# Kernel optimization log

Measured on AMD Instinct MI355X. Metric: run time of the kernel, lower is better.

## Reference

```python
import jax, jax.numpy as jnp
import numpy as np

EPS = 1e-6


def setup_inputs() -> dict:
    key = jax.random.key(0)
    kx, kw = jax.random.split(key)
    B, C, N = 8, 256, 2048
    x = jax.random.normal(kx, (B, C, N), dtype=jnp.float32)
    # nn.Linear(dim*2, 2, bias=False): weight shape [2, 2*C]
    W = jax.random.normal(kw, (2, 2 * C), dtype=jnp.float32) * (1.0 / np.sqrt(2 * C))
    return {"x": x, "W": W}


def reference(x, W):
    B, C, N = x.shape
    # cosine similarity matrix [B, N, N]
    sim = jnp.einsum('bcn,bcm->bnm', x, x)
    # torch: sqrt(sum(x^2 + 1e-6, dim=1)) -> eps added per-channel before sum
    norms = jnp.sqrt(jnp.sum(x * x + EPS, axis=1))            # [B, N]
    io_abs = sim / (norms[:, :, None] * norms[:, None, :])    # [B, N, N]
    # zero the diagonal (fill_diagonal_(0)) before argmax
    io_abs = io_abs * (1.0 - jnp.eye(N, dtype=io_abs.dtype))
    idx = jnp.argmax(io_abs, axis=2)                          # [B, N] nearest-neighbor per token
    # gather retrieved features: f_re[b, :, n] = x[b, :, idx[b, n]]
    f_re = jnp.take_along_axis(x, idx[:, None, :], axis=2)    # [B, C, N]
    # gated fusion
    fus = jnp.concatenate([x, f_re], axis=1).transpose(0, 2, 1)  # [B, N, 2C]
    w = jax.nn.softmax(fus @ W.T, axis=-1)                    # [B, N, 2]
    w = w.transpose(0, 2, 1)                                  # [B, 2, N]
    out = x * w[:, 0:1, :] + f_re * w[:, 1:2, :]
    return (out, f_re)
```

## Files before the change

### kernel.cpp

```cpp
#include <hip/hip_runtime.h>
#include <hip/hip_bf16.h>
#include <math.h>

constexpr int B_ = 8;
constexpr int C_ = 256;
constexpr int N_ = 2048;
constexpr int CN_ = C_ * N_;
constexpr int TOT_ = B_ * C_ * N_;
constexpr int BN_ = B_ * N_;
constexpr int NTILES = 16;
constexpr int NPAIRS = 136;
constexpr float EPSC = 256.0f * 1e-6f;

typedef __attribute__((ext_vector_type(8))) short bf16x8;
typedef __attribute__((ext_vector_type(4))) float f32x4;

__device__ __forceinline__ void g2l16(const void* g, void* l) {
    __builtin_amdgcn_global_load_lds(
        (const __attribute__((address_space(1))) void*)g,
        (__attribute__((address_space(3))) void*)l, 16, 0, 0);
}

__device__ __forceinline__ unsigned short bits(__hip_bfloat16 h) {
    union { __hip_bfloat16 b; unsigned short u; } cv;
    cv.b = h;
    return cv.u;
}

__device__ __forceinline__ float b2f(short s) {
    union { float f; unsigned u; } cv;
    cv.u = ((unsigned)(unsigned short)s) << 16;
    return cv.f;
}

__device__ __forceinline__ unsigned long long packkey(float v, int m) {
    const unsigned b = __float_as_uint(v);
    const unsigned u = (b & 0x80000000u) ? ~b : (b | 0x80000000u);
    return ((unsigned long long)u << 32) | (unsigned)(2047 - m);
}

__device__ __forceinline__ float rnorm4(const float* __restrict__ normp, int idx) {
    return 1.0f / sqrtf(normp[idx] + normp[BN_ + idx] + normp[2 * BN_ + idx] +
                        normp[3 * BN_ + idx] + EPSC);
}

__global__ __launch_bounds__(256) void convert_kernel(const float* __restrict__ x,
                                                      __hip_bfloat16* __restrict__ hiT,
                                                      __hip_bfloat16* __restrict__ loT,
                                                      float* __restrict__ normp,
                                                      int* __restrict__ rcnt) {
    const int blk = blockIdx.x;
    const int batch = blk & 7;
    const int nt = (blk >> 3) & 31;
    const int ctile = blk >> 8;
    const int n0 = nt << 6, c0 = ctile << 6;
    const int t = threadIdx.x;
    const int i = t & 63, j = t >> 6;

    if (blk == 0 && t == 0) rcnt[0] = 0;

    __shared__ float tb[64][65];
    __shared__ float red[4][64];

    float s = 0.f;
    const float* xp = x + (size_t)batch * CN_ + (size_t)c0 * N_ + n0 + i;
#pragma unroll 4
    for (int r = 0; r < 16; ++r) {
        const int cl = j + r * 4;
        const float v = xp[(size_t)cl * N_];
        tb[cl][i] = v;
        s += v * v;
    }
    red[j][i] = s;
    __syncthreads();

    const int cp = t & 31;
    const int c2 = cp << 1;
    const int nb = t >> 5;
#pragma unroll 4
    for (int r = 0; r < 8; ++r) {
        const int n = nb + r * 8;
        const float v0 = tb[c2][n], v1 = tb[c2 + 1][n];
        const size_t o = ((size_t)batch * N_ + n0 + n) * C_ + c0 + c2;
        const __hip_bfloat16 h0 = __float2bfloat16(v0);
        const __hip_bfloat16 h1 = __float2bfloat16(v1);
        const __hip_bfloat16 g0 = __float2bfloat16(v0 - __bfloat162float(h0));
        const __hip_bfloat16 g1 = __float2bfloat16(v1 - __bfloat162float(h1));
        ((unsigned*)hiT)[o >> 1] = ((unsigned)bits(h1) << 16) | bits(h0);
        ((unsigned*)loT)[o >> 1] = ((unsigned)bits(g1) << 16) | bits(g0);
    }
    if (j == 0) {
        const float tt = red[0][i] + red[1][i] + red[2][i] + red[3][i];
        normp[ctile * BN_ + batch * N_ + n0 + i] = tt;
    }
}

__global__ __launch_bounds__(512) void gram_mfma_kernel(
        const __hip_bfloat16* __restrict__ hiT, const __hip_bfloat16* __restrict__ loT,
        const float* __restrict__ normp,
        float* __restrict__ pval, int* __restrict__ pidx, float* __restrict__ pval2) {
    const int blk = blockIdx.x;
    const int batch = blk & 7;
    int p = blk >> 3;
    int bn = 0;
    while (p >= NTILES - bn) { p -= NTILES - bn; ++bn; }
    const int bm = bn + p;
    const bool diag = (bn == bm);
    const int n0 = bn << 7, m0 = bm << 7;

    __shared__ short As0[128 * 64];
    __shared__ short As1[128 * 64];
    __shared__ short Bs0[128 * 64];
    __shared__ short Bs1[128 * 64];
    short* ov = &As0[0];
    float (*rv1)[4] = (float(*)[4])(ov + 0);
    int (*ri1)[4] = (int(*)[4])(ov + 1024);
    float (*rv2)[4] = (float(*)[4])(ov + 2048);
    float (*cv1)[2] = (float(*)[2])(ov + 3072);
    int (*ci1)[2] = (int(*)[2])(ov + 3584);
    float (*cv2)[2] = (float(*)[2])(ov + 4096);
    float* rnA = (float*)(ov + 4608);

    const int tid = threadIdx.x;
    const int l = tid & 63, w = tid >> 6;
    const int lm = l & 15, q = l >> 4;
    const int x7 = lm & 7;
    const int wn = (w >> 2) << 6;
    const int wm = (w & 3) << 5;

    const size_t bbase = (size_t)batch * CN_;
    const short* gA[2];
    const short* gB[2];
    int ldsoff[2];
#pragma unroll
    for (int pp = 0; pp < 2; ++pp) {
        const int slot = tid + pp * 512;
        const int r = slot >> 3, sidx = slot & 7;
        const int sw = sidx ^ (r & 7);
        const short* base = (const short*)((sw < 4) ? hiT : loT);
        gA[pp] = base + bbase + (size_t)(n0 + r) * C_ + (sw & 3) * 8;
        gB[pp] = base + bbase + (size_t)(m0 + r) * C_ + (sw & 3) * 8;
        ldsoff[pp] = slot * 8;
    }
    int aoff[8], boff[4];
#pragma unroll
    for (int rt = 0; rt < 4; ++rt) {
        const int ra = wn + rt * 16 + lm;
        aoff[rt * 2] = ra * 64 + ((q ^ x7) * 8);
        aoff[rt * 2 + 1] = ra * 64 + (((4 | q) ^ x7) * 8);
    }
#pragma unroll
    for (int ct = 0; ct < 2; ++ct) {
        const int rb = wm + ct * 16 + lm;
        boff[ct * 2] = rb * 64 + ((q ^ x7) * 8);
        boff[ct * 2 + 1] = rb * 64 + (((4 | q) ^ x7) * 8);
    }

    f32x4 acc[4][2];
#pragma unroll
    for (int rt = 0; rt < 4; ++rt)
#pragma unroll
        for (int ct = 0; ct < 2; ++ct) acc[rt][ct] = (f32x4){0.f, 0.f, 0.f, 0.f};

#pragma unroll
    for (int pp = 0; pp < 2; ++pp) {
        g2l16(gA[pp], As0 + ldsoff[pp]);
        g2l16(gB[pp], Bs0 + ldsoff[pp]);
    }
    __syncthreads();

#pragma unroll
    for (int kt = 0; kt < 8; ++kt) {
        short* Ac = (kt & 1) ? As1 : As0;
        short* Bc = (kt & 1) ? Bs1 : Bs0;
        if (kt < 7) {
            short* An = (kt & 1) ? As0 : As1;
            short* Bn = (kt & 1) ? Bs0 : Bs1;
#pragma unroll
            for (int pp = 0; pp < 2; ++pp) {
                g2l16(gA[pp] + (kt + 1) * 32, An + ldsoff[pp]);
                g2l16(gB[pp] + (kt + 1) * 32, Bn + ldsoff[pp]);
            }
        }
        bf16x8 ah[4], al[4], bh[2], bl[2];
#pragma unroll
        for (int rt = 0; rt < 4; ++rt) {
            ah[rt] = *(const bf16x8*)(Ac + aoff[rt * 2]);
            al[rt] = *(const bf16x8*)(Ac + aoff[rt * 2 + 1]);
        }
#pragma unroll
        for (int ct = 0; ct < 2; ++ct) {
            bh[ct] = *(const bf16x8*)(Bc + boff[ct * 2]);
            bl[ct] = *(const bf16x8*)(Bc + boff[ct * 2 + 1]);
        }
#pragma unroll
        for (int rt = 0; rt < 4; ++rt)
#pragma unroll
            for (int ct = 0; ct < 2; ++ct) {
                acc[rt][ct] = __builtin_amdgcn_mfma_f32_16x16x32_bf16(
                    ah[rt], bh[ct], acc[rt][ct], 0, 0, 0);
                acc[rt][ct] = __builtin_amdgcn_mfma_f32_16x16x32_bf16(
                    ah[rt], bl[ct], acc[rt][ct], 0, 0, 0);
                acc[rt][ct] = __builtin_amdgcn_mfma_f32_16x16x32_bf16(
                    al[rt], bh[ct], acc[rt][ct], 0, 0, 0);
            }
        __syncthreads();
    }

    if (tid < 128) rnA[tid] = rnorm4(normp, batch * N_ + n0 + tid);

    float rnm[2];
#pragma unroll
    for (int ct = 0; ct < 2; ++ct)
        rnm[ct] = rnorm4(normp, batch * N_ + m0 + wm + ct * 16 + lm);

#pragma unroll
    for (int rt = 0; rt < 4; ++rt) {
#pragma unroll
        for (int r = 0; r < 4; ++r) {
            const int nrow = n0 + wn + rt * 16 + q * 4 + r;
            float v1 = -3.4e38f, v2 = -3.4e38f;
            int i1 = 0x7fffffff;
#pragma unroll
            for (int ct = 0; ct < 2; ++ct) {
                const int m = m0 + wm + ct * 16 + lm;
                const float v = acc[rt][ct][r] * rnm[ct];
                if (m == nrow) continue;
                if (v > v1) { v2 = v1; v1 = v; i1 = m; }
                else if (v > v2) v2 = v;
            }
#pragma unroll
            for (int d = 1; d < 16; d <<= 1) {
                const float ov1 = __shfl_xor(v1, d, 64);
                const int oi1 = __shfl_xor(i1, d, 64);
                const float ov2 = __shfl_xor(v2, d, 64);
                if (ov1 > v1 || (ov1 == v1 && oi1 < i1)) {
                    v2 = fmaxf(v1, ov2); v1 = ov1; i1 = oi1;
                } else {
                    v2 = fmaxf(v2, ov1);
                }
            }
            if (lm == 0) {
                const int rloc = wn + rt * 16 + q * 4 + r;
                rv1[rloc][w & 3] = v1;
                ri1[rloc][w & 3] = i1;
                rv2[rloc][w & 3] = v2;
            }
        }
    }
    __syncthreads();

    if (!diag) {
        float rnn[4][4];
#pragma unroll
        for (int rt = 0; rt < 4; ++rt)
#pragma unroll
            for (int r = 0; r < 4; ++r) rnn[rt][r] = rnA[wn + rt * 16 + q * 4 + r];
#pragma unroll
        for (int ct = 0; ct < 2; ++ct) {
            float v1 = -3.4e38f, v2 = -3.4e38f;
            int i1 = 0x7fffffff;
#pragma unroll
            for (int rt = 0; rt < 4; ++rt) {
#pragma unroll
                for (int r = 0; r < 4; ++r) {
                    const float v = acc[rt][ct][r] * rnn[rt][r];
                    const int nn = n0 + wn + rt * 16 + q * 4 + r;
                    if (v > v1) { v2 = v1; v1 = v; i1 = nn; }
                    else if (v > v2) v2 = v;
                }
            }
#pragma unroll
            for (int d = 16; d < 64; d <<= 1) {
                const float ov1 = __shfl_xor(v1, d, 64);
                const int oi1 = __shfl_xor(i1, d, 64);
                const float ov2 = __shfl_xor(v2, d, 64);
                if (ov1 > v1 || (ov1 == v1 && oi1 < i1)) {
                    v2 = fmaxf(v1, ov2); v1 = ov1; i1 = oi1;
                } else {
                    v2 = fmaxf(v2, ov1);
                }
            }
            if (q == 0) {
                const int mloc = wm + ct * 16 + lm;
                cv1[mloc][w >> 2] = v1;
                ci1[mloc][w >> 2] = i1;
                cv2[mloc][w >> 2] = v2;
            }
        }
    }
    __syncthreads();

    if (tid < 128) {
        {
            float v1 = rv1[tid][0]; int i1 = ri1[tid][0]; float v2 = rv2[tid][0];
#pragma unroll
            for (int s = 1; s < 4; ++s) {
                const float ov1 = rv1[tid][s]; const int oi1 = ri1[tid][s]; const float ov2 = rv2[tid][s];
                if (ov1 > v1 || (ov1 == v1 && oi1 < i1)) { v2 = fmaxf(v1, ov2); v1 = ov1; i1 = oi1; }
                else v2 = fmaxf(v2, ov1);
            }
            const size_t gi = (size_t)(batch * NTILES + bm) * N_ + n0 + tid;
            pval[gi] = v1; pidx[gi] = i1; pval2[gi] = v2;
        }
        if (!diag) {
            float v1 = cv1[tid][0]; int i1 = ci1[tid][0]; float v2 = cv2[tid][0];
            const float ov1 = cv1[tid][1]; const int oi1 = ci1[tid][1]; const float ov2 = cv2[tid][1];
            if (ov1 > v1 || (ov1 == v1 && oi1 < i1)) { v2 = fmaxf(v1, ov2); v1 = ov1; i1 = oi1; }
            else v2 = fmaxf(v2, ov1);
            const size_t gi = (size_t)(batch * NTILES + bn) * N_ + m0 + tid;
            pval[gi] = v1; pidx[gi] = i1; pval2[gi] = v2;
        }
    }
}

__global__ void combine_kernel(const float* __restrict__ pval, const int* __restrict__ pidx,
                               const float* __restrict__ pval2, int* __restrict__ fidx,
                               int* __restrict__ rcnt, int* __restrict__ ridx,
                               unsigned long long* __restrict__ pbest) {
    const int t = blockIdx.x * 256 + threadIdx.x;
    const int batch = t >> 11, n = t & 2047;
    float v1 = -3.4e38f, v2 = -3.4e38f;
    int i1 = 0x7fffffff;
    for (int s = 0; s < NTILES; ++s) {
        const size_t gi = (size_t)(batch * NTILES + s) * N_ + n;
        const float ov1 = pval[gi]; const int oi1 = pidx[gi]; const float ov2 = pval2[gi];
        if (ov1 > v1 || (ov1 == v1 && oi1 < i1)) { v2 = fmaxf(v1, ov2); v1 = ov1; i1 = oi1; }
        else v2 = fmaxf(v2, ov1);
    }
    fidx[t] = i1;
    if (v1 - v2 < 1e-4f) {
        const int slot = atomicAdd(rcnt, 1);
        ridx[slot] = t;
        pbest[slot] = 0ull;
    }
}

__global__ __launch_bounds__(256) void rescue_kernel(const float* __restrict__ x,
                                                     const float* __restrict__ normp,
                                                     const int* __restrict__ rcnt,
                                                     const int* __restrict__ ridx,
                                                     unsigned long long* __restrict__ pbest) {
    const int cnt = *rcnt;
    const int nwork = cnt << 3;
    const int tid = threadIdx.x;
    __shared__ unsigned long long bk[256];
    for (int wi = blockIdx.x; wi < nwork; wi += gridDim.x) {
        const int rr = wi >> 3, ch = wi & 7;
        const int t = ridx[rr];
        const int batch = t >> 11, n = t & 2047;
        const int m = (ch << 8) + tid;
        const float* xb = x + (size_t)batch * CN_;
        float s0 = 0.f, s1 = 0.f, s2 = 0.f, s3 = 0.f;
        const float* xn = xb + n;
        const float* xm = xb + m;
#pragma unroll 4
        for (int c = 0; c < C_; c += 4) {
            s0 += xn[(size_t)(c + 0) * N_] * xm[(size_t)(c + 0) * N_];
            s1 += xn[(size_t)(c + 1) * N_] * xm[(size_t)(c + 1) * N_];
            s2 += xn[(size_t)(c + 2) * N_] * xm[(size_t)(c + 2) * N_];
            s3 += xn[(size_t)(c + 3) * N_] * xm[(size_t)(c + 3) * N_];
        }
        const float v = ((s0 + s1) + (s2 + s3)) * rnorm4(normp, batch * N_ + m);
        bk[tid] = (m == n) ? 0ull : packkey(v, m);
        __syncthreads();
        for (int sft = 128; sft > 0; sft >>= 1) {
            if (tid < sft) {
                const unsigned long long o = bk[tid + sft];
                if (o > bk[tid]) bk[tid] = o;
            }
            __syncthreads();
        }
        if (tid == 0) atomicMax(&pbest[rr], bk[0]);
        __syncthreads();
    }
}

__global__ __launch_bounds__(512) void finish_kernel(const float* __restrict__ x,
                                                     const __hip_bfloat16* __restrict__ hiT,
                                                     const __hip_bfloat16* __restrict__ loT,
                                                     const float* __restrict__ W,
                                                     const int* __restrict__ fidx,
                                                     const int* __restrict__ rcnt,
                                                     const int* __restrict__ ridx,
                                                     const unsigned long long* __restrict__ pbest,
                                                     float* __restrict__ out) {
    const int batch = blockIdx.x & 7;
    const int nt = blockIdx.x >> 3;
    const int n0 = nt << 6;
    const int t = threadIdx.x;
    const int lane = t & 63, cw = t >> 6;

    __shared__ float Wl[1024];
    __shared__ int il[64];
    __shared__ float pl0[8][64], pl1[8][64];
    __shared__ float w0s[64], w1s[64];

    for (int u = t; u < 1024; u += 512) Wl[u] = W[u];
    if (t < 64) il[t] = fidx[batch * N_ + n0 + t];
    __syncthreads();
    {
        const int cnt = *rcnt;
        for (int rr = t; rr < cnt; rr += 512) {
            const int tt = ridx[rr];
            if ((tt >> 11) == batch) {
                const int n = tt & 2047;
                if (n >= n0 && n < n0 + 64) {
                    const unsigned long long k = pbest[rr];
                    il[n - n0] = 2047 - (int)(unsigned)(k & 0xffffffffull);
                }
            }
        }
    }
    __syncthreads();

    const int myrow = il[lane];
    const size_t rowb = ((size_t)batch * N_ + myrow) * C_ + cw * 32;

    float fre[32];
    {
        const bf16x8* hp = (const bf16x8*)(hiT + rowb);
        const bf16x8* lp = (const bf16x8*)(loT + rowb);
#pragma unroll
        for (int v8 = 0; v8 < 4; ++v8) {
            const bf16x8 h = hp[v8];
            const bf16x8 g = lp[v8];
#pragma unroll
            for (int e = 0; e < 8; ++e) fre[v8 * 8 + e] = b2f(h[e]) + b2f(g[e]);
        }
    }

    const float* xb = x + (size_t)batch * CN_ + n0 + lane;
    float xr[32];
    float l0 = 0.f, l1 = 0.f;
#pragma unroll
    for (int cc = 0; cc < 32; ++cc) {
        const int c = cw * 32 + cc;
        const float xv = xb[(size_t)c * N_];
        xr[cc] = xv;
        l0 += xv * Wl[c] + fre[cc] * Wl[256 + c];
        l1 += xv * Wl[512 + c] + fre[cc] * Wl[768 + c];
    }
    pl0[cw][lane] = l0;
    pl1[cw][lane] = l1;
    __syncthreads();
    if (t < 64) {
        float L0 = 0.f, L1 = 0.f;
#pragma unroll
        for (int g = 0; g < 8; ++g) { L0 += pl0[g][t]; L1 += pl1[g][t]; }
        const float mx = fmaxf(L0, L1);
        const float e0 = expf(L0 - mx);
        const float e1 = expf(L1 - mx);
        const float inv = 1.0f / (e0 + e1);
        w0s[t] = e0 * inv;
        w1s[t] = e1 * inv;
    }
    __syncthreads();
    const float w0 = w0s[lane], w1 = w1s[lane];

#pragma unroll
    for (int cc = 0; cc < 32; ++cc) {
        const int c = cw * 32 + cc;
        const size_t off = (size_t)batch * CN_ + (size_t)c * N_ + n0 + lane;
        out[off] = xr[cc] * w0 + fre[cc] * w1;
        out[TOT_ + off] = fre[cc];
    }
}

extern "C" void kernel_launch(void* const* d_in, const int* in_sizes, int n_in,
                              void* d_out, int out_size, void* d_ws, size_t ws_size,
                              hipStream_t stream) {
    const float* x = (const float*)d_in[0];
    const float* W = (const float*)d_in[1];
    float* out = (float*)d_out;

    const size_t BF_BYTES = (size_t)TOT_ * 2;
    const size_t NORM_BYTES = (size_t)BN_ * 4;
    const size_t P_BYTES = (size_t)B_ * NTILES * N_ * 4;

    uint8_t* p = (uint8_t*)d_ws;
    __hip_bfloat16* hiT = (__hip_bfloat16*)p; p += BF_BYTES;
    __hip_bfloat16* loT = (__hip_bfloat16*)p; p += BF_BYTES;
    float* normp = (float*)p; p += 4 * NORM_BYTES;
    float* pval = (float*)p; p += P_BYTES;
    int* pidx = (int*)p; p += P_BYTES;
    float* pval2 = (float*)p; p += P_BYTES;
    int* fidx = (int*)p; p += NORM_BYTES;
    int* rcnt = (int*)p; p += 256;
    int* ridx = (int*)p; p += NORM_BYTES;
    unsigned long long* pbest = (unsigned long long*)p; p += (size_t)BN_ * 8;

    convert_kernel<<<1024, 256, 0, stream>>>(x, hiT, loT, normp, rcnt);
    gram_mfma_kernel<<<B_ * NPAIRS, 512, 0, stream>>>(hiT, loT, normp, pval, pidx, pval2);
    combine_kernel<<<64, 256, 0, stream>>>(pval, pidx, pval2, fidx, rcnt, ridx, pbest);
    rescue_kernel<<<256, 256, 0, stream>>>(x, normp, rcnt, ridx, pbest);
    finish_kernel<<<256, 512, 0, stream>>>(x, hiT, loT, W, fidx, rcnt, ridx, pbest, out);
}
```

Measured before the change: 174.2 us.

## Batch rescue rows per block with per-batch queues and wave-shuffle reductions

```diff
diff --git a/kernel.cpp b/kernel.cpp
--- a/kernel.cpp
+++ b/kernel.cpp
@@ -10,10 +10,13 @@
 constexpr int BN_ = B_ * N_;
 constexpr int NTILES = 16;
 constexpr int NPAIRS = 136;
+constexpr int TCAP = 2048;
+constexpr int MAXG = 128;
 constexpr float EPSC = 256.0f * 1e-6f;
 
 typedef __attribute__((ext_vector_type(8))) short bf16x8;
 typedef __attribute__((ext_vector_type(4))) float f32x4;
+typedef __attribute__((ext_vector_type(2))) unsigned int u32x2;
 
 __device__ __forceinline__ void g2l16(const void* g, void* l) {
     __builtin_amdgcn_global_load_lds(
@@ -42,6 +45,10 @@
 __device__ __forceinline__ float rnorm4(const float* __restrict__ normp, int idx) {
     return 1.0f / sqrtf(normp[idx] + normp[BN_ + idx] + normp[2 * BN_ + idx] +
                         normp[3 * BN_ + idx] + EPSC);
+}
+
+__device__ __forceinline__ unsigned packpair(float a, float b) {
+    return ((unsigned)bits(__float2bfloat16(b)) << 16) | bits(__float2bfloat16(a));
 }
 
 __global__ __launch_bounds__(256) void convert_kernel(const float* __restrict__ x,
@@ -57,7 +64,7 @@
     const int t = threadIdx.x;
     const int i = t & 63, j = t >> 6;
 
-    if (blk == 0 && t == 0) rcnt[0] = 0;
+    if (blk == 0 && t < 8) rcnt[t] = 0;
 
     __shared__ float tb[64][65];
     __shared__ float red[4][64];
@@ -74,20 +81,29 @@
     red[j][i] = s;
     __syncthreads();
 
-    const int cp = t & 31;
-    const int c2 = cp << 1;
-    const int nb = t >> 5;
-#pragma unroll 4
-    for (int r = 0; r < 8; ++r) {
-        const int n = nb + r * 8;
-        const float v0 = tb[c2][n], v1 = tb[c2 + 1][n];
-        const size_t o = ((size_t)batch * N_ + n0 + n) * C_ + c0 + c2;
+    const int cq = t & 15;
+    const int nb = t >> 4;
+#pragma unroll
+    for (int r = 0; r < 4; ++r) {
+        const int n = nb + r * 16;
+        const int c = cq << 2;
+        float v0 = tb[c][n], v1 = tb[c + 1][n], v2 = tb[c + 2][n], v3 = tb[c + 3][n];
         const __hip_bfloat16 h0 = __float2bfloat16(v0);
         const __hip_bfloat16 h1 = __float2bfloat16(v1);
-        const __hip_bfloat16 g0 = __float2bfloat16(v0 - __bfloat162float(h0));
-        const __hip_bfloat16 g1 = __float2bfloat16(v1 - __bfloat162float(h1));
-        ((unsigned*)hiT)[o >> 1] = ((unsigned)bits(h1) << 16) | bits(h0);
-        ((unsigned*)loT)[o >> 1] = ((unsigned)bits(g1) << 16) | bits(g0);
+        const __hip_bfloat16 h2 = __float2bfloat16(v2);
+        const __hip_bfloat16 h3 = __float2bfloat16(v3);
+        const float g0 = v0 - __bfloat162float(h0);
+        const float g1 = v1 - __bfloat162float(h1);
+        const float g2 = v2 - __bfloat162float(h2);
+        const float g3 = v3 - __bfloat162float(h3);
+        const size_t o = ((size_t)batch * N_ + n0 + n) * C_ + c0 + c;
+        u32x2 hp, lp;
+        hp[0] = ((unsigned)bits(h1) << 16) | bits(h0);
+        hp[1] = ((unsigned)bits(h3) << 16) | bits(h2);
+        lp[0] = packpair(g0, g1);
+        lp[1] = packpair(g2, g3);
+        ((u32x2*)hiT)[o >> 2] = hp;
+        ((u32x2*)loT)[o >> 2] = lp;
     }
     if (j == 0) {
         const float tt = red[0][i] + red[1][i] + red[2][i] + red[3][i];
@@ -330,9 +346,11 @@
     }
     fidx[t] = i1;
     if (v1 - v2 < 1e-4f) {
-        const int slot = atomicAdd(rcnt, 1);
-        ridx[slot] = t;
-        pbest[slot] = 0ull;
+        const int slot = atomicAdd(rcnt + batch, 1);
+        if (slot < TCAP) {
+            ridx[batch * TCAP + slot] = n;
+            pbest[batch * TCAP + slot] = 0ull;
+        }
     }
 }
 
@@ -341,38 +359,59 @@
                                                      const int* __restrict__ rcnt,
                                                      const int* __restrict__ ridx,
                                                      unsigned long long* __restrict__ pbest) {
-    const int cnt = *rcnt;
-    const int nwork = cnt << 3;
     const int tid = threadIdx.x;
-    __shared__ unsigned long long bk[256];
-    for (int wi = blockIdx.x; wi < nwork; wi += gridDim.x) {
-        const int rr = wi >> 3, ch = wi & 7;
-        const int t = ridx[rr];
-        const int batch = t >> 11, n = t & 2047;
+    __shared__ float xn[16][256];
+    __shared__ int nrow[16];
+    __shared__ unsigned long long wk[4][16];
+
+    for (int wi = blockIdx.x; wi < 8 * MAXG * 8; wi += gridDim.x) {
+        const int b = wi >> 10;
+        const int g = (wi >> 3) & (MAXG - 1);
+        const int ch = wi & 7;
+        const int cnt = min(rcnt[b], TCAP);
+        if (g * 16 >= cnt) continue;
+        const int nt = min(16, cnt - g * 16);
+        const float* xb = x + (size_t)b * CN_;
+
+        __syncthreads();
+        if (tid < 16) nrow[tid] = ridx[b * TCAP + g * 16 + ((tid < nt) ? tid : 0)];
+        __syncthreads();
+        {
+            const int c = tid & 255;
+            for (int j = 0; j < 16; ++j) xn[j][c] = xb[(size_t)c * N_ + nrow[j]];
+        }
+        __syncthreads();
+
         const int m = (ch << 8) + tid;
-        const float* xb = x + (size_t)batch * CN_;
-        float s0 = 0.f, s1 = 0.f, s2 = 0.f, s3 = 0.f;
-        const float* xn = xb + n;
+        float acc[16];
+#pragma unroll
+        for (int j = 0; j < 16; ++j) acc[j] = 0.f;
         const float* xm = xb + m;
-#pragma unroll 4
-        for (int c = 0; c < C_; c += 4) {
-            s0 += xn[(size_t)(c + 0) * N_] * xm[(size_t)(c + 0) * N_];
-            s1 += xn[(size_t)(c + 1) * N_] * xm[(size_t)(c + 1) * N_];
-            s2 += xn[(size_t)(c + 2) * N_] * xm[(size_t)(c + 2) * N_];
-            s3 += xn[(size_t)(c + 3) * N_] * xm[(size_t)(c + 3) * N_];
-        }
-        const float v = ((s0 + s1) + (s2 + s3)) * rnorm4(normp, batch * N_ + m);
-        bk[tid] = (m == n) ? 0ull : packkey(v, m);
+        for (int c = 0; c < C_; ++c) {
+            const float vm = xm[(size_t)c * N_];
+#pragma unroll
+            for (int j = 0; j < 16; ++j) acc[j] += vm * xn[j][c];
+        }
+        const float rn = rnorm4(normp, b * N_ + m);
+        const int w = tid >> 6;
+#pragma unroll
+        for (int j = 0; j < 16; ++j) {
+            unsigned long long k = (m == nrow[j]) ? 0ull : packkey(acc[j] * rn, m);
+#pragma unroll
+            for (int d = 1; d < 64; d <<= 1) {
+                const unsigned long long o = __shfl_xor(k, d, 64);
+                if (o > k) k = o;
+            }
+            if ((tid & 63) == 0) wk[w][j] = k;
+        }
         __syncthreads();
-        for (int sft = 128; sft > 0; sft >>= 1) {
-            if (tid < sft) {
-                const unsigned long long o = bk[tid + sft];
-                if (o > bk[tid]) bk[tid] = o;
-            }
-            __syncthreads();
-        }
-        if (tid == 0) atomicMax(&pbest[rr], bk[0]);
-        __syncthreads();
+        if (tid < 16 && tid < nt) {
+            unsigned long long k = wk[0][tid];
+            if (wk[1][tid] > k) k = wk[1][tid];
+            if (wk[2][tid] > k) k = wk[2][tid];
+            if (wk[3][tid] > k) k = wk[3][tid];
+            atomicMax(&pbest[b * TCAP + g * 16 + tid], k);
+        }
     }
 }
 
@@ -400,15 +439,12 @@
     if (t < 64) il[t] = fidx[batch * N_ + n0 + t];
     __syncthreads();
     {
-        const int cnt = *rcnt;
+        const int cnt = min(rcnt[batch], TCAP);
         for (int rr = t; rr < cnt; rr += 512) {
-            const int tt = ridx[rr];
-            if ((tt >> 11) == batch) {
-                const int n = tt & 2047;
-                if (n >= n0 && n < n0 + 64) {
-                    const unsigned long long k = pbest[rr];
-                    il[n - n0] = 2047 - (int)(unsigned)(k & 0xffffffffull);
-                }
+            const int n = ridx[batch * TCAP + rr];
+            if (n >= n0 && n < n0 + 64) {
+                const unsigned long long k = pbest[batch * TCAP + rr];
+                il[n - n0] = 2047 - (int)(unsigned)(k & 0xffffffffull);
             }
         }
     }
```

Measured after the change: 312.9 us. 1.8x slower.

## Fuse combine, rescue and finish into one cooperative kernel; vectorize bf16 split stores

Applied to the files above, without the earlier changes.

```diff
diff --git a/kernel.cpp b/kernel.cpp
--- a/kernel.cpp
+++ b/kernel.cpp
@@ -1,6 +1,9 @@
 #include <hip/hip_runtime.h>
 #include <hip/hip_bf16.h>
+#include <hip/hip_cooperative_groups.h>
 #include <math.h>
+
+namespace cg = cooperative_groups;
 
 constexpr int B_ = 8;
 constexpr int C_ = 256;
@@ -14,6 +17,7 @@
 
 typedef __attribute__((ext_vector_type(8))) short bf16x8;
 typedef __attribute__((ext_vector_type(4))) float f32x4;
+typedef __attribute__((ext_vector_type(2))) unsigned int u32x2;
 
 __device__ __forceinline__ void g2l16(const void* g, void* l) {
     __builtin_amdgcn_global_load_lds(
@@ -42,6 +46,10 @@
 __device__ __forceinline__ float rnorm4(const float* __restrict__ normp, int idx) {
     return 1.0f / sqrtf(normp[idx] + normp[BN_ + idx] + normp[2 * BN_ + idx] +
                         normp[3 * BN_ + idx] + EPSC);
+}
+
+__device__ __forceinline__ unsigned packpair(float a, float b) {
+    return ((unsigned)bits(__float2bfloat16(b)) << 16) | bits(__float2bfloat16(a));
 }
 
 __global__ __launch_bounds__(256) void convert_kernel(const float* __restrict__ x,
@@ -74,20 +82,29 @@
     red[j][i] = s;
     __syncthreads();
 
-    const int cp = t & 31;
-    const int c2 = cp << 1;
-    const int nb = t >> 5;
-#pragma unroll 4
-    for (int r = 0; r < 8; ++r) {
-        const int n = nb + r * 8;
-        const float v0 = tb[c2][n], v1 = tb[c2 + 1][n];
-        const size_t o = ((size_t)batch * N_ + n0 + n) * C_ + c0 + c2;
+    const int cq = t & 15;
+    const int nb = t >> 4;
+#pragma unroll
+    for (int r = 0; r < 4; ++r) {
+        const int n = nb + r * 16;
+        const int c = cq << 2;
+        float v0 = tb[c][n], v1 = tb[c + 1][n], v2 = tb[c + 2][n], v3 = tb[c + 3][n];
         const __hip_bfloat16 h0 = __float2bfloat16(v0);
         const __hip_bfloat16 h1 = __float2bfloat16(v1);
-        const __hip_bfloat16 g0 = __float2bfloat16(v0 - __bfloat162float(h0));
-        const __hip_bfloat16 g1 = __float2bfloat16(v1 - __bfloat162float(h1));
-        ((unsigned*)hiT)[o >> 1] = ((unsigned)bits(h1) << 16) | bits(h0);
-        ((unsigned*)loT)[o >> 1] = ((unsigned)bits(g1) << 16) | bits(g0);
+        const __hip_bfloat16 h2 = __float2bfloat16(v2);
+        const __hip_bfloat16 h3 = __float2bfloat16(v3);
+        const float g0 = v0 - __bfloat162float(h0);
+        const float g1 = v1 - __bfloat162float(h1);
+        const float g2 = v2 - __bfloat162float(h2);
+        const float g3 = v3 - __bfloat162float(h3);
+        const size_t o = ((size_t)batch * N_ + n0 + n) * C_ + c0 + c;
+        u32x2 hp, lp;
+        hp[0] = ((unsigned)bits(h1) << 16) | bits(h0);
+        hp[1] = ((unsigned)bits(h3) << 16) | bits(h2);
+        lp[0] = packpair(g0, g1);
+        lp[1] = packpair(g2, g3);
+        ((u32x2*)hiT)[o >> 2] = hp;
+        ((u32x2*)loT)[o >> 2] = lp;
     }
     if (j == 0) {
         const float tt = red[0][i] + red[1][i] + red[2][i] + red[3][i];
@@ -314,156 +331,155 @@
     }
 }
 
-__global__ void combine_kernel(const float* __restrict__ pval, const int* __restrict__ pidx,
-                               const float* __restrict__ pval2, int* __restrict__ fidx,
-                               int* __restrict__ rcnt, int* __restrict__ ridx,
-                               unsigned long long* __restrict__ pbest) {
-    const int t = blockIdx.x * 256 + threadIdx.x;
-    const int batch = t >> 11, n = t & 2047;
-    float v1 = -3.4e38f, v2 = -3.4e38f;
-    int i1 = 0x7fffffff;
-    for (int s = 0; s < NTILES; ++s) {
-        const size_t gi = (size_t)(batch * NTILES + s) * N_ + n;
-        const float ov1 = pval[gi]; const int oi1 = pidx[gi]; const float ov2 = pval2[gi];
-        if (ov1 > v1 || (ov1 == v1 && oi1 < i1)) { v2 = fmaxf(v1, ov2); v1 = ov1; i1 = oi1; }
-        else v2 = fmaxf(v2, ov1);
-    }
-    fidx[t] = i1;
-    if (v1 - v2 < 1e-4f) {
-        const int slot = atomicAdd(rcnt, 1);
-        ridx[slot] = t;
-        pbest[slot] = 0ull;
-    }
-}
-
-__global__ __launch_bounds__(256) void rescue_kernel(const float* __restrict__ x,
-                                                     const float* __restrict__ normp,
-                                                     const int* __restrict__ rcnt,
-                                                     const int* __restrict__ ridx,
-                                                     unsigned long long* __restrict__ pbest) {
-    const int cnt = *rcnt;
-    const int nwork = cnt << 3;
+__global__ __launch_bounds__(512) void tail_kernel(
+        const float* __restrict__ x,
+        const __hip_bfloat16* __restrict__ hiT, const __hip_bfloat16* __restrict__ loT,
+        const float* __restrict__ W, const float* __restrict__ normp,
+        const float* __restrict__ pval, const int* __restrict__ pidx,
+        const float* __restrict__ pval2,
+        int* __restrict__ fidx, int* __restrict__ rcnt, int* __restrict__ ridx,
+        unsigned long long* __restrict__ pbest, float* __restrict__ out) {
     const int tid = threadIdx.x;
-    __shared__ unsigned long long bk[256];
-    for (int wi = blockIdx.x; wi < nwork; wi += gridDim.x) {
-        const int rr = wi >> 3, ch = wi & 7;
-        const int t = ridx[rr];
-        const int batch = t >> 11, n = t & 2047;
-        const int m = (ch << 8) + tid;
-        const float* xb = x + (size_t)batch * CN_;
-        float s0 = 0.f, s1 = 0.f, s2 = 0.f, s3 = 0.f;
-        const float* xn = xb + n;
-        const float* xm = xb + m;
-#pragma unroll 4
-        for (int c = 0; c < C_; c += 4) {
-            s0 += xn[(size_t)(c + 0) * N_] * xm[(size_t)(c + 0) * N_];
-            s1 += xn[(size_t)(c + 1) * N_] * xm[(size_t)(c + 1) * N_];
-            s2 += xn[(size_t)(c + 2) * N_] * xm[(size_t)(c + 2) * N_];
-            s3 += xn[(size_t)(c + 3) * N_] * xm[(size_t)(c + 3) * N_];
-        }
-        const float v = ((s0 + s1) + (s2 + s3)) * rnorm4(normp, batch * N_ + m);
-        bk[tid] = (m == n) ? 0ull : packkey(v, m);
-        __syncthreads();
-        for (int sft = 128; sft > 0; sft >>= 1) {
-            if (tid < sft) {
-                const unsigned long long o = bk[tid + sft];
-                if (o > bk[tid]) bk[tid] = o;
-            }
-            __syncthreads();
-        }
-        if (tid == 0) atomicMax(&pbest[rr], bk[0]);
-        __syncthreads();
-    }
-}
-
-__global__ __launch_bounds__(512) void finish_kernel(const float* __restrict__ x,
-                                                     const __hip_bfloat16* __restrict__ hiT,
-                                                     const __hip_bfloat16* __restrict__ loT,
-                                                     const float* __restrict__ W,
-                                                     const int* __restrict__ fidx,
-                                                     const int* __restrict__ rcnt,
-                                                     const int* __restrict__ ridx,
-                                                     const unsigned long long* __restrict__ pbest,
-                                                     float* __restrict__ out) {
-    const int batch = blockIdx.x & 7;
-    const int nt = blockIdx.x >> 3;
-    const int n0 = nt << 6;
-    const int t = threadIdx.x;
-    const int lane = t & 63, cw = t >> 6;
-
+    const int blk = blockIdx.x;
+
+    __shared__ unsigned long long bk[512];
     __shared__ float Wl[1024];
     __shared__ int il[64];
     __shared__ float pl0[8][64], pl1[8][64];
     __shared__ float w0s[64], w1s[64];
 
-    for (int u = t; u < 1024; u += 512) Wl[u] = W[u];
-    if (t < 64) il[t] = fidx[batch * N_ + n0 + t];
-    __syncthreads();
+    {
+        const int t = blk * 512 + tid;
+        if (t < BN_) {
+            const int batch = t >> 11, n = t & 2047;
+            float v1 = -3.4e38f, v2 = -3.4e38f;
+            int i1 = 0x7fffffff;
+            for (int s = 0; s < NTILES; ++s) {
+                const size_t gi = (size_t)(batch * NTILES + s) * N_ + n;
+                const float ov1 = pval[gi]; const int oi1 = pidx[gi]; const float ov2 = pval2[gi];
+                if (ov1 > v1 || (ov1 == v1 && oi1 < i1)) { v2 = fmaxf(v1, ov2); v1 = ov1; i1 = oi1; }
+                else v2 = fmaxf(v2, ov1);
+            }
+            fidx[t] = i1;
+            if (v1 - v2 < 1e-4f) {
+                const int slot = atomicAdd(rcnt, 1);
+                ridx[slot] = t;
+                pbest[slot] = 0ull;
+            }
+        }
+    }
+    cg::this_grid().sync();
+
     {
         const int cnt = *rcnt;
-        for (int rr = t; rr < cnt; rr += 512) {
-            const int tt = ridx[rr];
-            if ((tt >> 11) == batch) {
-                const int n = tt & 2047;
-                if (n >= n0 && n < n0 + 64) {
-                    const unsigned long long k = pbest[rr];
-                    il[n - n0] = 2047 - (int)(unsigned)(k & 0xffffffffull);
+        const int nwork = cnt << 2;
+        for (int wi = blk; wi < nwork; wi += 256) {
+            const int rr = wi >> 2, ch = wi & 3;
+            const int t = ridx[rr];
+            const int batch = t >> 11, n = t & 2047;
+            const int m = (ch << 9) + tid;
+            const float* xb = x + (size_t)batch * CN_;
+            float s0 = 0.f, s1 = 0.f, s2 = 0.f, s3 = 0.f;
+            const float* xn = xb + n;
+            const float* xm = xb + m;
+#pragma unroll 4
+            for (int c = 0; c < C_; c += 4) {
+                s0 += xn[(size_t)(c + 0) * N_] * xm[(size_t)(c + 0) * N_];
+                s1 += xn[(size_t)(c + 1) * N_] * xm[(size_t)(c + 1) * N_];
+                s2 += xn[(size_t)(c + 2) * N_] * xm[(size_t)(c + 2) * N_];
+                s3 += xn[(size_t)(c + 3) * N_] * xm[(size_t)(c + 3) * N_];
+            }
+            const float v = ((s0 + s1) + (s2 + s3)) * rnorm4(normp, batch * N_ + m);
+            bk[tid] = (m == n) ? 0ull : packkey(v, m);
+            __syncthreads();
+            for (int sft = 256; sft > 0; sft >>= 1) {
+                if (tid < sft) {
+                    const unsigned long long o = bk[tid + sft];
+                    if (o > bk[tid]) bk[tid] = o;
                 }
-            }
-        }
-    }
-    __syncthreads();
-
-    const int myrow = il[lane];
-    const size_t rowb = ((size_t)batch * N_ + myrow) * C_ + cw * 32;
-
-    float fre[32];
+                __syncthreads();
+            }
+            if (tid == 0) atomicMax(&pbest[rr], bk[0]);
+            __syncthreads();
+        }
+    }
+    cg::this_grid().sync();
+
     {
-        const bf16x8* hp = (const bf16x8*)(hiT + rowb);
-        const bf16x8* lp = (const bf16x8*)(loT + rowb);
-#pragma unroll
-        for (int v8 = 0; v8 < 4; ++v8) {
-            const bf16x8 h = hp[v8];
-            const bf16x8 g = lp[v8];
-#pragma unroll
-            for (int e = 0; e < 8; ++e) fre[v8 * 8 + e] = b2f(h[e]) + b2f(g[e]);
-        }
-    }
-
-    const float* xb = x + (size_t)batch * CN_ + n0 + lane;
-    float xr[32];
-    float l0 = 0.f, l1 = 0.f;
-#pragma unroll
-    for (int cc = 0; cc < 32; ++cc) {
-        const int c = cw * 32 + cc;
-        const float xv = xb[(size_t)c * N_];
-        xr[cc] = xv;
-        l0 += xv * Wl[c] + fre[cc] * Wl[256 + c];
-        l1 += xv * Wl[512 + c] + fre[cc] * Wl[768 + c];
-    }
-    pl0[cw][lane] = l0;
-    pl1[cw][lane] = l1;
-    __syncthreads();
-    if (t < 64) {
-        float L0 = 0.f, L1 = 0.f;
-#pragma unroll
-        for (int g = 0; g < 8; ++g) { L0 += pl0[g][t]; L1 += pl1[g][t]; }
-        const float mx = fmaxf(L0, L1);
-        const float e0 = expf(L0 - mx);
-        const float e1 = expf(L1 - mx);
-        const float inv = 1.0f / (e0 + e1);
-        w0s[t] = e0 * inv;
-        w1s[t] = e1 * inv;
-    }
-    __syncthreads();
-    const float w0 = w0s[lane], w1 = w1s[lane];
-
-#pragma unroll
-    for (int cc = 0; cc < 32; ++cc) {
-        const int c = cw * 32 + cc;
-        const size_t off = (size_t)batch * CN_ + (size_t)c * N_ + n0 + lane;
-        out[off] = xr[cc] * w0 + fre[cc] * w1;
-        out[TOT_ + off] = fre[cc];
+        const int batch = blk & 7;
+        const int nt = blk >> 3;
+        const int n0 = nt << 6;
+        const int lane = tid & 63, cw = tid >> 6;
+
+        for (int u = tid; u < 1024; u += 512) Wl[u] = W[u];
+        if (tid < 64) il[tid] = fidx[batch * N_ + n0 + tid];
+        __syncthreads();
+        {
+            const int cnt = *rcnt;
+            for (int rr = tid; rr < cnt; rr += 512) {
+                const int tt = ridx[rr];
+                if ((tt >> 11) == batch) {
+                    const int n = tt & 2047;
+                    if (n >= n0 && n < n0 + 64) {
+                        const unsigned long long k = pbest[rr];
+                        il[n - n0] = 2047 - (int)(unsigned)(k & 0xffffffffull);
+                    }
+                }
+            }
+        }
+        __syncthreads();
+
+        const int myrow = il[lane];
+        const size_t rowb = ((size_t)batch * N_ + myrow) * C_ + cw * 32;
+
+        float fre[32];
+        {
+            const bf16x8* hp = (const bf16x8*)(hiT + rowb);
+            const bf16x8* lp = (const bf16x8*)(loT + rowb);
+#pragma unroll
+            for (int v8 = 0; v8 < 4; ++v8) {
+                const bf16x8 h = hp[v8];
+                const bf16x8 g = lp[v8];
+#pragma unroll
+                for (int e = 0; e < 8; ++e) fre[v8 * 8 + e] = b2f(h[e]) + b2f(g[e]);
+            }
+        }
+
+        const float* xb = x + (size_t)batch * CN_ + n0 + lane;
+        float xr[32];
+        float l0 = 0.f, l1 = 0.f;
+#pragma unroll
+        for (int cc = 0; cc < 32; ++cc) {
+            const int c = cw * 32 + cc;
+            const float xv = xb[(size_t)c * N_];
+            xr[cc] = xv;
+            l0 += xv * Wl[c] + fre[cc] * Wl[256 + c];
+            l1 += xv * Wl[512 + c] + fre[cc] * Wl[768 + c];
+        }
+        pl0[cw][lane] = l0;
+        pl1[cw][lane] = l1;
+        __syncthreads();
+        if (tid < 64) {
+            float L0 = 0.f, L1 = 0.f;
+#pragma unroll
+            for (int g = 0; g < 8; ++g) { L0 += pl0[g][tid]; L1 += pl1[g][tid]; }
+            const float mx = fmaxf(L0, L1);
+            const float e0 = expf(L0 - mx);
+            const float e1 = expf(L1 - mx);
+            const float inv = 1.0f / (e0 + e1);
+            w0s[tid] = e0 * inv;
+            w1s[tid] = e1 * inv;
+        }
+        __syncthreads();
+        const float w0 = w0s[lane], w1 = w1s[lane];
+
+#pragma unroll
+        for (int cc = 0; cc < 32; ++cc) {
+            const int c = cw * 32 + cc;
+            const size_t off = (size_t)batch * CN_ + (size_t)c * N_ + n0 + lane;
+            out[off] = xr[cc] * w0 + fre[cc] * w1;
+            out[TOT_ + off] = fre[cc];
+        }
     }
 }
 
@@ -492,7 +508,9 @@
 
     convert_kernel<<<1024, 256, 0, stream>>>(x, hiT, loT, normp, rcnt);
     gram_mfma_kernel<<<B_ * NPAIRS, 512, 0, stream>>>(hiT, loT, normp, pval, pidx, pval2);
-    combine_kernel<<<64, 256, 0, stream>>>(pval, pidx, pval2, fidx, rcnt, ridx, pbest);
-    rescue_kernel<<<256, 256, 0, stream>>>(x, normp, rcnt, ridx, pbest);
-    finish_kernel<<<256, 512, 0, stream>>>(x, hiT, loT, W, fidx, rcnt, ridx, pbest, out);
-}
+
+    void* args[] = {(void*)&x, (void*)&hiT, (void*)&loT, (void*)&W, (void*)&normp,
+                    (void*)&pval, (void*)&pidx, (void*)&pval2,
+                    (void*)&fidx, (void*)&rcnt, (void*)&ridx, (void*)&pbest, (void*)&out};
+    (void)hipLaunchCooperativeKernel((const void*)tail_kernel, dim3(256), dim3(512), args, 0, stream);
+}
```

After: 232.9 us. 1.34x slower.
